# Performance work log

Measured on AMD Instinct MI355X. Metric: run time of the kernel, lower is better.

## Reference

```python
import jax, jax.numpy as jnp
import numpy as np

B, T, C = 16, 2048, 256
TT = T  # maxlen
LAYER_ID, N_LAYER = 3, 6


def setup_inputs() -> dict:
    key = jax.random.key(0)
    ks = jax.random.split(key, 6)
    ratio_0_to_1 = LAYER_ID / (N_LAYER - 1)
    ratio_1_to_almost0 = 1.0 - LAYER_ID / N_LAYER

    h = np.arange(TT, dtype=np.float32)
    decay_speed = -5.0 + 8.0 * (h / (TT - 1)) ** (0.7 + 1.3 * ratio_0_to_1)
    curve = -(TT - 1 - h)  # curve[i] = -(maxlen-1-i)
    # Faithful init ww = exp(curve * decay_speed); clip exponent so the table
    # stays finite (raw init overflows to inf for large maxlen; time_w is a
    # learned parameter, so finite plausible values are appropriate).
    time_w = jnp.asarray(np.exp(np.clip(curve * decay_speed, -30.0, 0.0)), dtype=jnp.float32)

    i = np.arange(C, dtype=np.float32) / C  # x[0,0,i] = i / hidden_units
    time_mix_k = jnp.asarray((i ** ratio_1_to_almost0).reshape(1, 1, C), dtype=jnp.float32)
    time_mix_v = jnp.asarray((i ** ratio_1_to_almost0 + 0.3 * ratio_0_to_1).reshape(1, 1, C), dtype=jnp.float32)
    time_mix_r = jnp.asarray((i ** (0.5 * ratio_1_to_almost0)).reshape(1, 1, C), dtype=jnp.float32)

    x = jax.random.normal(ks[0], (B, T, C), dtype=jnp.float32)
    scale = 0.02
    Wk = scale * jax.random.normal(ks[1], (C, C), dtype=jnp.float32)
    Wv = scale * jax.random.normal(ks[2], (C, C), dtype=jnp.float32)
    Wr = scale * jax.random.normal(ks[3], (C, C), dtype=jnp.float32)
    Wo = scale * jax.random.normal(ks[4], (C, C), dtype=jnp.float32)
    return {"x": x, "time_w": time_w, "time_mix_k": time_mix_k,
            "time_mix_v": time_mix_v, "time_mix_r": time_mix_r,
            "Wk": Wk, "Wv": Wv, "Wr": Wr, "Wo": Wo}


def reference(x, time_w, time_mix_k, time_mix_v, time_mix_r, Wk, Wv, Wr, Wo):
    Bx, Tx, Cx = x.shape
    maxlen = time_w.shape[0]
    # time_shift: shift sequence right by one, zero-pad the first step
    xx = jnp.pad(x, ((0, 0), (1, 0), (0, 0)))[:, :-1]
    xk = x * time_mix_k + xx * (1.0 - time_mix_k)
    xv = x * time_mix_v + xx * (1.0 - time_mix_v)
    xr = x * time_mix_r + xx * (1.0 - time_mix_r)

    k = jnp.exp(jnp.clip(xk @ Wk, -60.0, 30.0))  # [B,T,C]
    v = xv @ Wv
    r = xr @ Wr

    sum_k = jnp.cumsum(k, axis=1)
    kv = k * v

    # Toeplitz decay matrix: W[t,u] = time_w[maxlen-1-(t-u)] for u<=t, else 0
    t_idx = jnp.arange(Tx)
    d = t_idx[:, None] - t_idx[None, :]  # lag t-u
    W = jnp.where(d >= 0, time_w[jnp.clip(maxlen - 1 - d, 0, maxlen - 1)], 0.0)

    wkv = jnp.einsum('tu,buc->btc', W, kv)  # O(T^2 * C) WKV mixing
    rwkv = jax.nn.sigmoid(r) * wkv / sum_k
    return rwkv @ Wo
```

## Files before the change

kernel.cpp:

```cpp
#include <hip/hip_runtime.h>
#include <hip/hip_bf16.h>

#define NB 16
#define NT 2048
#define NC 256
#define NM (NB*NT)
#define NCH 16
#define NCL (NT/NCH)

typedef __attribute__((ext_vector_type(8))) short short8;
typedef __attribute__((ext_vector_type(4))) float f32x4;

__device__ __forceinline__ unsigned short f2bf(float x){
    union { float f; unsigned u; } v; v.f = x;
    unsigned r = v.u + 0x7FFFu + ((v.u >> 16) & 1u);
    return (unsigned short)(r >> 16);
}
__device__ __forceinline__ float bf2f(unsigned short x){
    union { unsigned u; float f; } v; v.u = ((unsigned)x) << 16;
    return v.f;
}
__device__ __forceinline__ void gload16(const unsigned short* g, unsigned short* l){
    __builtin_amdgcn_global_load_lds((const __attribute__((address_space(1))) void*)g,
                                     (__attribute__((address_space(3))) void*)l, 16, 0, 0);
}


__global__ void prep_kernel(const float* __restrict__ tw,
                            const float* __restrict__ Wk, const float* __restrict__ Wv,
                            const float* __restrict__ Wr, const float* __restrict__ Wo,
                            unsigned short* __restrict__ WkT, unsigned short* __restrict__ WvT,
                            unsigned short* __restrict__ WrT, unsigned short* __restrict__ WoT,
                            unsigned short* __restrict__ Aexp){
    int gid = blockIdx.x*256 + threadIdx.x;
    {
        int n = gid >> 8, u = gid & 255;
        int usw = (u & ~63) | ((((u>>3)&7) ^ (n&7)) << 3) | (u & 7);
        int src = u*NC + n;
        WkT[n*NC + usw] = f2bf(Wk[src]);
        WvT[n*NC + usw] = f2bf(Wv[src]);
        WrT[n*NC + usw] = f2bf(Wr[src]);
        WoT[n*NC + usw] = f2bf(Wo[src]);
    }
    if (gid < 32768){
        int Di = gid >> 10, rem = gid & 1023;
        int r = rem >> 3, ql = rem & 7;
        int qlog = ql ^ (r & 7);
        int D = Di*64 - 1920;
        short8 vv;
        #pragma unroll
        for (int j = 0; j < 8; j++){
            int idx = 2047 + D - r + qlog*8 + j;
            float val = (idx >= 0 && idx < NT) ? tw[idx] : 0.f;
            vv[j] = (short)f2bf(val);
        }
        *(short8*)&Aexp[(size_t)gid*8] = vv;
    }
}

__global__ void mix_kernel(const float* __restrict__ x,
                           const float* __restrict__ tmk, const float* __restrict__ tmv,
                           const float* __restrict__ tmr,
                           unsigned short* __restrict__ xk, unsigned short* __restrict__ xv,
                           unsigned short* __restrict__ xr){
    int gid = blockIdx.x*256 + threadIdx.x;
    int m = gid >> 5;
    int c0 = (gid & 31) << 3;
    int t = m & (NT-1);
    size_t base = (size_t)m*NC + c0;
    float xa[8], xb[8];
    #pragma unroll
    for (int j=0;j<8;j+=4) *(float4*)&xa[j] = *(const float4*)&x[base+j];
    if (t > 0) {
        #pragma unroll
        for (int j=0;j<8;j+=4) *(float4*)&xb[j] = *(const float4*)&x[base - NC + j];
    } else {
        #pragma unroll
        for (int j=0;j<8;j++) xb[j]=0.f;
    }
    short8 ok, ov, orr;
    #pragma unroll
    for (int j=0;j<8;j++){
        float mk = tmk[c0+j], mv = tmv[c0+j], mr = tmr[c0+j];
        ok[j]  = (short)f2bf(xa[j]*mk + xb[j]*(1.f-mk));
        ov[j]  = (short)f2bf(xa[j]*mv + xb[j]*(1.f-mv));
        orr[j] = (short)f2bf(xa[j]*mr + xb[j]*(1.f-mr));
    }
    int csw = (c0 & ~63) | ((((c0>>3)&7) ^ (m&7)) << 3);
    size_t dst = (size_t)m*NC + csw;
    *(short8*)&xk[dst] = ok;
    *(short8*)&xv[dst] = ov;
    *(short8*)&xr[dst] = orr;
}

template<int MODE>
__global__ __launch_bounds__(256) void gemm_c(const unsigned short* __restrict__ A,
                                              const unsigned short* __restrict__ BT,
                                              void* __restrict__ outp){
    __shared__ unsigned short As[2][128*64];
    __shared__ unsigned short Bs[2][128*64];
    const int tid = threadIdx.x;
    const int lane = tid & 63, w = tid >> 6;
    const int wm = (w >> 1) * 64, wn = (w & 1) * 64;
    const int m0 = blockIdx.x * 128, n0 = blockIdx.y * 128;
    const int lrow = lane & 15, kgrp = lane >> 4, lx = lane & 7;
    const int qrow = tid >> 3, qc = tid & 7;

    f32x4 acc[4][4] = {};

    auto STAGE = [&](int buf, int k0){
        #pragma unroll
        for (int i=0;i<4;i++){
            int row = qrow + 32*i;
            int q = row*8 + qc;
            gload16(A  + (size_t)(m0+row)*NC + k0 + qc*8, &As[buf][q*8]);
            gload16(BT + (size_t)(n0+row)*NC + k0 + qc*8, &Bs[buf][q*8]);
        }
    };

    STAGE(0, 0);
    __syncthreads();
    for (int s = 0; s < 4; ++s){
        if (s < 3) STAGE((s+1)&1, (s+1)*64);
        const unsigned short* as = As[s&1];
        const unsigned short* bs = Bs[s&1];
        #pragma unroll
        for (int ks = 0; ks < 2; ++ks){
            const int lk = ks*4 + kgrp;
            const int ch = (lk ^ lx) << 3;
            short8 a[4], b[4];
            #pragma unroll
            for (int mi=0;mi<4;mi++) a[mi] = *(const short8*)&as[(wm + mi*16 + lrow)*64 + ch];
            #pragma unroll
            for (int ni=0;ni<4;ni++) b[ni] = *(const short8*)&bs[(wn + ni*16 + lrow)*64 + ch];
            #pragma unroll
            for (int mi=0;mi<4;mi++)
            #pragma unroll
            for (int ni=0;ni<4;ni++)
                acc[mi][ni] = __builtin_amdgcn_mfma_f32_16x16x32_bf16(a[mi], b[ni], acc[mi][ni], 0,0,0);
        }
        __syncthreads();
    }

    const int orow = m0 + wm + kgrp*4;
    const int ocol = n0 + wn + lrow;
    #pragma unroll
    for (int mi=0;mi<4;mi++)
    #pragma unroll
    for (int ni=0;ni<4;ni++)
    #pragma unroll
    for (int i=0;i<4;i++){
        float vv = acc[mi][ni][i];
        size_t off = (size_t)(orow + mi*16 + i)*NC + ocol + ni*16;
        if (MODE == 0) ((float*)outp)[off] = vv;
        if (MODE == 1) ((float*)outp)[off] = __expf(fminf(fmaxf(vv,-60.f),30.f));
        if (MODE == 2) ((unsigned short*)outp)[off] = f2bf(vv);
        if (MODE == 3) ((unsigned short*)outp)[off] = f2bf(1.f/(1.f+__expf(-vv)));
    }
}

__global__ __launch_bounds__(256) void kv_kernel(const float* __restrict__ kf,
                                                 const unsigned short* __restrict__ vb,
                                                 unsigned short* __restrict__ kvt){
    __shared__ unsigned short tile[64][65];
    const int tx = blockIdx.x*64, cx = blockIdx.y*64, b = blockIdx.z;
    const int tid = threadIdx.x;
    {
        int r = tid >> 2, c0 = (tid & 3) * 16;
        size_t base = ((size_t)(b*NT + tx + r))*NC + cx + c0;
        short8 v8a = *(const short8*)&vb[base];
        short8 v8b = *(const short8*)&vb[base+8];
        #pragma unroll
        for (int j=0;j<16;j+=4){
            float4 k4 = *(const float4*)&kf[base+j];
            float f0 = (j<8)? bf2f((unsigned short)v8a[j&7])   : bf2f((unsigned short)v8b[j&7]);
            float f1 = (j<8)? bf2f((unsigned short)v8a[(j&7)+1]) : bf2f((unsigned short)v8b[(j&7)+1]);
            float f2 = (j<8)? bf2f((unsigned short)v8a[(j&7)+2]) : bf2f((unsigned short)v8b[(j&7)+2]);
            float f3 = (j<8)? bf2f((unsigned short)v8a[(j&7)+3]) : bf2f((unsigned short)v8b[(j&7)+3]);
            tile[r][c0+j+0] = f2bf(k4.x*f0);
            tile[r][c0+j+1] = f2bf(k4.y*f1);
            tile[r][c0+j+2] = f2bf(k4.z*f2);
            tile[r][c0+j+3] = f2bf(k4.w*f3);
        }
    }
    __syncthreads();
    #pragma unroll
    for (int rep=0;rep<2;rep++){
        int row = (tid >> 3) + rep*32;
        int cs = (tid & 7) * 8;
        short8 vv;
        #pragma unroll
        for (int j=0;j<8;j++) vv[j] = (short)tile[cs+j][row];
        int csw = ((cs>>3) ^ (row&7)) << 3;
        *(short8*)&kvt[((size_t)(b*NC + cx + row))*NT + tx + csw] = vv;
    }
}

__global__ void scan1(const float* __restrict__ kf, float* __restrict__ part){
    int gid = blockIdx.x*256 + threadIdx.x;
    int c = gid & 255, ch = (gid >> 8) & 15, b = gid >> 12;
    const float* p = kf + ((size_t)b*NT + ch*NCL)*NC + c;
    float s = 0.f;
    for (int i=0;i<NCL;i++) s += p[(size_t)i*NC];
    part[gid] = s;
}
__global__ void scan2(const float* __restrict__ kf, const float* __restrict__ part,
                      float* __restrict__ sumk){
    int gid = blockIdx.x*256 + threadIdx.x;
    int c = gid & 255, ch = (gid >> 8) & 15, b = gid >> 12;
    float off = 0.f;
    for (int j=0;j<ch;j++) off += part[((b*NCH + j)<<8) + c];
    const float* p = kf + ((size_t)b*NT + ch*NCL)*NC + c;
    float* o = sumk + ((size_t)b*NT + ch*NCL)*NC + c;
    float s = off;
    for (int i=0;i<NCL;i++){ s += p[(size_t)i*NC]; o[(size_t)i*NC] = s; }
}

__global__ __launch_bounds__(256) void gemm_wkv(const unsigned short* __restrict__ Aexp,
                                                const unsigned short* __restrict__ kvt,
                                                const unsigned short* __restrict__ srb,
                                                const float* __restrict__ sumk,
                                                unsigned short* __restrict__ rout){
    __shared__ unsigned short As[2][128*64];
    __shared__ unsigned short Bs[2][128*64];
    const int tid = threadIdx.x;
    const int lane = tid & 63, w = tid >> 6;
    const int wm = (w >> 1) * 64, wn = (w & 1) * 64;
    const int lrow = lane & 15, kgrp = lane >> 4, lx = lane & 7;
    const int qrow = tid >> 3, qc = tid & 7;

    const int id = blockIdx.x;
    const int j = id & 255, hi = id >> 8;
    const int t_idx = hi ? (15 - (j >> 4)) : (j >> 4);
    const int cb = (j & 15) | (hi << 4);
    const int c0 = (cb & 1) * 128;
    const int b  = cb >> 1;
    const int t0 = t_idx * 128;
    const int nsteps = t_idx*2 + 2;
    const unsigned short* Ab = Aexp + (size_t)(30 - 2*t_idx)*8192;

    f32x4 acc[4][4] = {};

    auto STAGE = [&](int buf, int s){
        const int u0 = s*64;
        #pragma unroll
        for (int i=0;i<4;i++){
            int row = qrow + 32*i;
            int q = row*8 + qc;
            gload16(Ab + (size_t)s*8192 + (size_t)q*8, &As[buf][q*8]);
            gload16(kvt + ((size_t)b*NC + c0 + row)*NT + u0 + qc*8, &Bs[buf][q*8]);
        }
    };

    STAGE(0, 0);
    __syncthreads();
    for (int s = 0; s < nsteps; ++s){
        if (s+1 < nsteps) STAGE((s+1)&1, s+1);
        const unsigned short* as = As[s&1];
        const unsigned short* bs = Bs[s&1];
        #pragma unroll
        for (int ks = 0; ks < 2; ++ks){
            const int lk = ks*4 + kgrp;
            const int ch = (lk ^ lx) << 3;
            short8 a[4], b8[4];
            #pragma unroll
            for (int mi=0;mi<4;mi++) a[mi]  = *(const short8*)&as[(wm + mi*16 + lrow)*64 + ch];
            #pragma unroll
            for (int ni=0;ni<4;ni++) b8[ni] = *(const short8*)&bs[(wn + ni*16 + lrow)*64 + ch];
            #pragma unroll
            for (int mi=0;mi<4;mi++)
            #pragma unroll
            for (int ni=0;ni<4;ni++)
                acc[mi][ni] = __builtin_amdgcn_mfma_f32_16x16x32_bf16(a[mi], b8[ni], acc[mi][ni], 0,0,0);
        }
        __syncthreads();
    }

    const int orow = wm + kgrp*4;
    const int ocol = c0 + wn + lrow;
    #pragma unroll
    for (int mi=0;mi<4;mi++)
    #pragma unroll
    for (int ni=0;ni<4;ni++)
    #pragma unroll
    for (int i=0;i<4;i++){
        int t = t0 + orow + mi*16 + i;
        int col = ocol + ni*16;
        size_t g = (size_t)(b*NT + t)*NC + col;
        float sr = bf2f(srb[g]);
        float sk = sumk[g];
        float vv = sr * acc[mi][ni][i] / sk;
        int csw = (col & ~63) | ((((col>>3)&7) ^ (t&7)) << 3) | (col & 7);
        rout[(size_t)(b*NT + t)*NC + csw] = f2bf(vv);
    }
}

extern "C" void kernel_launch(void* const* d_in, const int* in_sizes, int n_in,
                              void* d_out, int out_size, void* d_ws, size_t ws_size,
                              hipStream_t stream) {
    const float* x   = (const float*)d_in[0];
    const float* tw  = (const float*)d_in[1];
    const float* tmk = (const float*)d_in[2];
    const float* tmv = (const float*)d_in[3];
    const float* tmr = (const float*)d_in[4];
    const float* Wk  = (const float*)d_in[5];
    const float* Wv  = (const float*)d_in[6];
    const float* Wr  = (const float*)d_in[7];
    const float* Wo  = (const float*)d_in[8];

    char* ws = (char*)d_ws;
    const size_t MC = (size_t)NM*NC;
    unsigned short* xk   = (unsigned short*)(ws);
    unsigned short* xv   = (unsigned short*)(ws + MC*2);
    unsigned short* xr   = (unsigned short*)(ws + MC*4);
    float*          kf   = (float*)(ws + MC*6);
    unsigned short* vb   = (unsigned short*)(ws + MC*10);
    unsigned short* srb  = (unsigned short*)(ws + MC*12);
    float*          sumk = (float*)(ws + MC*14);
    unsigned short* kvt  = (unsigned short*)(ws + MC*18);
    unsigned short* Aexp = (unsigned short*)(ws + MC*20);
    unsigned short* WkT  = (unsigned short*)(ws + MC*20 + 524288);
    unsigned short* WvT  = WkT + NC*NC;
    unsigned short* WrT  = WvT + NC*NC;
    unsigned short* WoT  = WrT + NC*NC;
    float*          part = (float*)(ws + MC*20 + 1048576);
    unsigned short* rwkvb = xk;

    prep_kernel<<<256,256,0,stream>>>(tw, Wk,Wv,Wr,Wo, WkT,WvT,WrT,WoT, Aexp);
    mix_kernel<<<(int)(MC/8/256),256,0,stream>>>(x,tmk,tmv,tmr,xk,xv,xr);
    gemm_c<1><<<dim3(NM/128,NC/128),256,0,stream>>>(xk,WkT,kf);
    gemm_c<2><<<dim3(NM/128,NC/128),256,0,stream>>>(xv,WvT,vb);
    gemm_c<3><<<dim3(NM/128,NC/128),256,0,stream>>>(xr,WrT,srb);
    kv_kernel<<<dim3(NT/64,NC/64,NB),256,0,stream>>>(kf,vb,kvt);
    scan1<<<256,256,0,stream>>>(kf,part);
    scan2<<<256,256,0,stream>>>(kf,part,sumk);
    gemm_wkv<<<512,256,0,stream>>>(Aexp,kvt,srb,sumk,rwkvb);
    gemm_c<0><<<dim3(NM/128,NC/128),256,0,stream>>>(rwkvb,WoT,(float*)d_out);
}
```

Before: 141.2 us.

## Fuse k*v product and transpose into K GEMM epilogue; split WKV GEMM columns

The V projection now writes its bf16 output transposed (per batch, channel-major) through an LDS tile. The K projection epilogue reads that transposed V, computes exp(k)*v and writes the swizzled kvt layout directly, which removes the separate kv_kernel and its reread of k and v. Separately, the WKV GEMM switches from 128x128 to 128x64 output tiles and launches 1024 blocks, giving better load balance on the triangular workload. In exchange the A tiles are reloaded twice as often, and the transposing epilogues add an extra LDS pass.

```diff
diff --git a/kernel.cpp b/kernel.cpp
--- a/kernel.cpp
+++ b/kernel.cpp
@@ -9,6 +9,8 @@
 #define NCL (NT/NCH)
 
 typedef __attribute__((ext_vector_type(8))) short short8;
+typedef __attribute__((ext_vector_type(4))) short short4v;
+typedef __attribute__((ext_vector_type(4))) unsigned short ushort4v;
 typedef __attribute__((ext_vector_type(4))) float f32x4;
 
 __device__ __forceinline__ unsigned short f2bf(float x){
@@ -96,9 +98,12 @@
 template<int MODE>
 __global__ __launch_bounds__(256) void gemm_c(const unsigned short* __restrict__ A,
                                               const unsigned short* __restrict__ BT,
-                                              void* __restrict__ outp){
-    __shared__ unsigned short As[2][128*64];
-    __shared__ unsigned short Bs[2][128*64];
+                                              void* __restrict__ outp,
+                                              const unsigned short* __restrict__ vbT,
+                                              unsigned short* __restrict__ kvt){
+    __shared__ unsigned short smem[32768];
+    unsigned short* As0 = smem;
+    unsigned short* Bs0 = smem + 16384;
     const int tid = threadIdx.x;
     const int lane = tid & 63, w = tid >> 6;
     const int wm = (w >> 1) * 64, wn = (w & 1) * 64;
@@ -113,8 +118,8 @@
         for (int i=0;i<4;i++){
             int row = qrow + 32*i;
             int q = row*8 + qc;
-            gload16(A  + (size_t)(m0+row)*NC + k0 + qc*8, &As[buf][q*8]);
-            gload16(BT + (size_t)(n0+row)*NC + k0 + qc*8, &Bs[buf][q*8]);
+            gload16(A  + (size_t)(m0+row)*NC + k0 + qc*8, As0 + buf*8192 + q*8);
+            gload16(BT + (size_t)(n0+row)*NC + k0 + qc*8, Bs0 + buf*8192 + q*8);
         }
     };
 
@@ -122,8 +127,8 @@
     __syncthreads();
     for (int s = 0; s < 4; ++s){
         if (s < 3) STAGE((s+1)&1, (s+1)*64);
-        const unsigned short* as = As[s&1];
-        const unsigned short* bs = Bs[s&1];
+        const unsigned short* as = As0 + (s&1)*8192;
+        const unsigned short* bs = Bs0 + (s&1)*8192;
         #pragma unroll
         for (int ks = 0; ks < 2; ++ks){
             const int lk = ks*4 + kgrp;
@@ -142,57 +147,58 @@
         __syncthreads();
     }
 
-    const int orow = m0 + wm + kgrp*4;
-    const int ocol = n0 + wn + lrow;
-    #pragma unroll
-    for (int mi=0;mi<4;mi++)
-    #pragma unroll
-    for (int ni=0;ni<4;ni++)
-    #pragma unroll
-    for (int i=0;i<4;i++){
-        float vv = acc[mi][ni][i];
-        size_t off = (size_t)(orow + mi*16 + i)*NC + ocol + ni*16;
-        if (MODE == 0) ((float*)outp)[off] = vv;
-        if (MODE == 1) ((float*)outp)[off] = __expf(fminf(fmaxf(vv,-60.f),30.f));
-        if (MODE == 2) ((unsigned short*)outp)[off] = f2bf(vv);
-        if (MODE == 3) ((unsigned short*)outp)[off] = f2bf(1.f/(1.f+__expf(-vv)));
-    }
-}
-
-__global__ __launch_bounds__(256) void kv_kernel(const float* __restrict__ kf,
-                                                 const unsigned short* __restrict__ vb,
-                                                 unsigned short* __restrict__ kvt){
-    __shared__ unsigned short tile[64][65];
-    const int tx = blockIdx.x*64, cx = blockIdx.y*64, b = blockIdx.z;
-    const int tid = threadIdx.x;
-    {
-        int r = tid >> 2, c0 = (tid & 3) * 16;
-        size_t base = ((size_t)(b*NT + tx + r))*NC + cx + c0;
-        short8 v8a = *(const short8*)&vb[base];
-        short8 v8b = *(const short8*)&vb[base+8];
-        #pragma unroll
-        for (int j=0;j<16;j+=4){
-            float4 k4 = *(const float4*)&kf[base+j];
-            float f0 = (j<8)? bf2f((unsigned short)v8a[j&7])   : bf2f((unsigned short)v8b[j&7]);
-            float f1 = (j<8)? bf2f((unsigned short)v8a[(j&7)+1]) : bf2f((unsigned short)v8b[(j&7)+1]);
-            float f2 = (j<8)? bf2f((unsigned short)v8a[(j&7)+2]) : bf2f((unsigned short)v8b[(j&7)+2]);
-            float f3 = (j<8)? bf2f((unsigned short)v8a[(j&7)+3]) : bf2f((unsigned short)v8b[(j&7)+3]);
-            tile[r][c0+j+0] = f2bf(k4.x*f0);
-            tile[r][c0+j+1] = f2bf(k4.y*f1);
-            tile[r][c0+j+2] = f2bf(k4.z*f2);
-            tile[r][c0+j+3] = f2bf(k4.w*f3);
-        }
-    }
-    __syncthreads();
-    #pragma unroll
-    for (int rep=0;rep<2;rep++){
-        int row = (tid >> 3) + rep*32;
-        int cs = (tid & 7) * 8;
-        short8 vv;
-        #pragma unroll
-        for (int j=0;j<8;j++) vv[j] = (short)tile[cs+j][row];
-        int csw = ((cs>>3) ^ (row&7)) << 3;
-        *(short8*)&kvt[((size_t)(b*NC + cx + row))*NT + tx + csw] = vv;
+    const int orow = wm + kgrp*4;
+    const int ocol = wn + lrow;
+    if (MODE == 0 || MODE == 3){
+        #pragma unroll
+        for (int mi=0;mi<4;mi++)
+        #pragma unroll
+        for (int ni=0;ni<4;ni++)
+        #pragma unroll
+        for (int i=0;i<4;i++){
+            float vv = acc[mi][ni][i];
+            size_t off = (size_t)(m0 + orow + mi*16 + i)*NC + n0 + ocol + ni*16;
+            if (MODE == 0) ((float*)outp)[off] = vv;
+            if (MODE == 3) ((unsigned short*)outp)[off] = f2bf(1.f/(1.f+__expf(-vv)));
+        }
+    } else {
+        const int b = m0 >> 11, t0b = m0 & 2047;
+        unsigned short (*tileT)[136] = (unsigned short (*)[136])smem;
+        #pragma unroll
+        for (int mi=0;mi<4;mi++)
+        #pragma unroll
+        for (int ni=0;ni<4;ni++){
+            const int cL = ocol + ni*16;
+            const int t4 = orow + mi*16;
+            short4v pk;
+            if (MODE == 5){
+                ushort4v v4 = *(const ushort4v*)&vbT[((size_t)(b*NC + n0 + cL))*NT + t0b + t4];
+                #pragma unroll
+                for (int i=0;i<4;i++){
+                    float ke = __expf(fminf(fmaxf(acc[mi][ni][i],-60.f),30.f));
+                    ((float*)outp)[(size_t)(m0 + t4 + i)*NC + n0 + cL] = ke;
+                    pk[i] = (short)f2bf(ke * bf2f(v4[i]));
+                }
+            } else {
+                #pragma unroll
+                for (int i=0;i<4;i++) pk[i] = (short)f2bf(acc[mi][ni][i]);
+            }
+            *(short4v*)&tileT[cL][t4] = pk;
+        }
+        __syncthreads();
+        #pragma unroll
+        for (int p=0;p<8;p++){
+            int c = (tid >> 4) + p*16;
+            int t8 = (tid & 15) * 8;
+            short8 vv = *(const short8*)&tileT[c][t8];
+            if (MODE == 4){
+                *(short8*)&((unsigned short*)outp)[((size_t)(b*NC + n0 + c))*NT + t0b + t8] = vv;
+            } else {
+                int row = n0 + c;
+                int colp = (t8 & ~63) | ((((t8>>3)&7) ^ (row&7)) << 3);
+                *(short8*)&kvt[((size_t)(b*NC + row))*NT + t0b + colp] = vv;
+            }
+        }
     }
 }
 
@@ -222,33 +228,36 @@
                                                 const float* __restrict__ sumk,
                                                 unsigned short* __restrict__ rout){
     __shared__ unsigned short As[2][128*64];
-    __shared__ unsigned short Bs[2][128*64];
+    __shared__ unsigned short Bs[2][64*64];
     const int tid = threadIdx.x;
     const int lane = tid & 63, w = tid >> 6;
-    const int wm = (w >> 1) * 64, wn = (w & 1) * 64;
+    const int wm = (w >> 1) * 64, wn = (w & 1) * 32;
     const int lrow = lane & 15, kgrp = lane >> 4, lx = lane & 7;
     const int qrow = tid >> 3, qc = tid & 7;
 
     const int id = blockIdx.x;
-    const int j = id & 255, hi = id >> 8;
-    const int t_idx = hi ? (15 - (j >> 4)) : (j >> 4);
-    const int cb = (j & 15) | (hi << 4);
-    const int c0 = (cb & 1) * 128;
-    const int b  = cb >> 1;
+    const int j = id & 511, hi = id >> 9;
+    const int t_idx = hi ? 15 - (j >> 5) : (j >> 5);
+    const int combo = (j & 31) | (hi << 5);
+    const int b  = combo >> 2;
+    const int c0 = (combo & 3) * 64;
     const int t0 = t_idx * 128;
-    const int nsteps = t_idx*2 + 2;
+    const int nsteps = 2*t_idx + 2;
     const unsigned short* Ab = Aexp + (size_t)(30 - 2*t_idx)*8192;
 
-    f32x4 acc[4][4] = {};
+    f32x4 acc[4][2] = {};
 
     auto STAGE = [&](int buf, int s){
         const int u0 = s*64;
         #pragma unroll
         for (int i=0;i<4;i++){
             int row = qrow + 32*i;
-            int q = row*8 + qc;
-            gload16(Ab + (size_t)s*8192 + (size_t)q*8, &As[buf][q*8]);
-            gload16(kvt + ((size_t)b*NC + c0 + row)*NT + u0 + qc*8, &Bs[buf][q*8]);
+            gload16(Ab + (size_t)s*8192 + (size_t)(row*8+qc)*8, &As[buf][(row*8+qc)*8]);
+        }
+        #pragma unroll
+        for (int i=0;i<2;i++){
+            int row = qrow + 32*i;
+            gload16(kvt + ((size_t)(b*NC + c0 + row))*NT + u0 + qc*8, &Bs[buf][(row*8+qc)*8]);
         }
     };
 
@@ -262,15 +271,15 @@
         for (int ks = 0; ks < 2; ++ks){
             const int lk = ks*4 + kgrp;
             const int ch = (lk ^ lx) << 3;
-            short8 a[4], b8[4];
+            short8 a[4], b8[2];
             #pragma unroll
             for (int mi=0;mi<4;mi++) a[mi]  = *(const short8*)&as[(wm + mi*16 + lrow)*64 + ch];
             #pragma unroll
-            for (int ni=0;ni<4;ni++) b8[ni] = *(const short8*)&bs[(wn + ni*16 + lrow)*64 + ch];
+            for (int ni=0;ni<2;ni++) b8[ni] = *(const short8*)&bs[(wn + ni*16 + lrow)*64 + ch];
             #pragma unroll
             for (int mi=0;mi<4;mi++)
             #pragma unroll
-            for (int ni=0;ni<4;ni++)
+            for (int ni=0;ni<2;ni++)
                 acc[mi][ni] = __builtin_amdgcn_mfma_f32_16x16x32_bf16(a[mi], b8[ni], acc[mi][ni], 0,0,0);
         }
         __syncthreads();
@@ -281,7 +290,7 @@
     #pragma unroll
     for (int mi=0;mi<4;mi++)
     #pragma unroll
-    for (int ni=0;ni<4;ni++)
+    for (int ni=0;ni<2;ni++)
     #pragma unroll
     for (int i=0;i<4;i++){
         int t = t0 + orow + mi*16 + i;
@@ -314,7 +323,7 @@
     unsigned short* xv   = (unsigned short*)(ws + MC*2);
     unsigned short* xr   = (unsigned short*)(ws + MC*4);
     float*          kf   = (float*)(ws + MC*6);
-    unsigned short* vb   = (unsigned short*)(ws + MC*10);
+    unsigned short* vbT  = (unsigned short*)(ws + MC*10);
     unsigned short* srb  = (unsigned short*)(ws + MC*12);
     float*          sumk = (float*)(ws + MC*14);
     unsigned short* kvt  = (unsigned short*)(ws + MC*18);
@@ -328,12 +337,11 @@
 
     prep_kernel<<<256,256,0,stream>>>(tw, Wk,Wv,Wr,Wo, WkT,WvT,WrT,WoT, Aexp);
     mix_kernel<<<(int)(MC/8/256),256,0,stream>>>(x,tmk,tmv,tmr,xk,xv,xr);
-    gemm_c<1><<<dim3(NM/128,NC/128),256,0,stream>>>(xk,WkT,kf);
-    gemm_c<2><<<dim3(NM/128,NC/128),256,0,stream>>>(xv,WvT,vb);
-    gemm_c<3><<<dim3(NM/128,NC/128),256,0,stream>>>(xr,WrT,srb);
-    kv_kernel<<<dim3(NT/64,NC/64,NB),256,0,stream>>>(kf,vb,kvt);
+    gemm_c<4><<<dim3(NM/128,NC/128),256,0,stream>>>(xv,WvT,vbT,nullptr,nullptr);
+    gemm_c<5><<<dim3(NM/128,NC/128),256,0,stream>>>(xk,WkT,kf,vbT,kvt);
+    gemm_c<3><<<dim3(NM/128,NC/128),256,0,stream>>>(xr,WrT,srb,nullptr,nullptr);
     scan1<<<256,256,0,stream>>>(kf,part);
     scan2<<<256,256,0,stream>>>(kf,part,sumk);
-    gemm_wkv<<<512,256,0,stream>>>(Aexp,kvt,srb,sumk,rwkvb);
-    gemm_c<0><<<dim3(NM/128,NC/128),256,0,stream>>>(rwkvb,WoT,(float*)d_out);
-}
+    gemm_wkv<<<1024,256,0,stream>>>(Aexp,kvt,srb,sumk,rwkvb);
+    gemm_c<0><<<dim3(NM/128,NC/128),256,0,stream>>>(rwkvb,WoT,(float*)d_out,nullptr,nullptr);
+}
```

Measured after the change: 138.9 us. No clear change (-1.7%).
